# Optimization experiments

Measured on AMD Instinct MI355X. Metric: run time of the kernel, lower is better.

Reference implementation:

```python
import jax, jax.numpy as jnp
import numpy as np

N_HEAD = 12
N_EMBD = 768


def setup_inputs() -> dict:
    key = jax.random.key(0)
    ks = jax.random.split(key, 5)
    B, T, C = 8, 1024, N_EMBD
    x = jax.random.normal(ks[0], (B, T, C), dtype=jnp.float32)
    # c_attn: Linear(C, 3C); c_proj: Linear(C, C). PyTorch Linear: y = x @ W.T + b
    s = 1.0 / np.sqrt(C)
    W_attn = jax.random.uniform(ks[1], (3 * C, C), minval=-s, maxval=s, dtype=jnp.float32)
    b_attn = jax.random.uniform(ks[2], (3 * C,), minval=-s, maxval=s, dtype=jnp.float32)
    W_proj = jax.random.uniform(ks[3], (C, C), minval=-s, maxval=s, dtype=jnp.float32)
    b_proj = jax.random.uniform(ks[4], (C,), minval=-s, maxval=s, dtype=jnp.float32)
    return {"x": x, "W_attn": W_attn, "b_attn": b_attn, "W_proj": W_proj, "b_proj": b_proj}


def reference(x, W_attn, b_attn, W_proj, b_proj):
    B, T, C = x.shape
    H = N_HEAD
    hs = C // H  # head size
    qkv = x @ W_attn.T + b_attn  # [B, T, 3C]
    q, k, v = jnp.split(qkv, 3, axis=2)
    # [B, T, H, hs] -> [B, H, T, hs]
    q = q.reshape(B, T, H, hs).transpose(0, 2, 1, 3)
    k = k.reshape(B, T, H, hs).transpose(0, 2, 1, 3)
    v = v.reshape(B, T, H, hs).transpose(0, 2, 1, 3)
    att = jnp.einsum('bhqd,bhkd->bhqk', q, k) * (1.0 / np.sqrt(hs))
    causal = jnp.tril(jnp.ones((T, T), dtype=bool))
    att = jnp.where(causal, att, -jnp.inf)
    att = jax.nn.softmax(att, axis=-1)
    y = jnp.einsum('bhqk,bhkd->bhqd', att, v)  # [B, H, T, hs]
    y = y.transpose(0, 2, 1, 3).reshape(B, T, C)
    return y @ W_proj.T + b_proj
```

## Files before the change

kernel.cpp:

```cpp
#include <hip/hip_runtime.h>

typedef unsigned short u16;
typedef __attribute__((ext_vector_type(8))) __bf16 bf16x8;
typedef __attribute__((ext_vector_type(4))) float f32x4;
typedef __attribute__((ext_vector_type(4))) int i32x4;

#define MFMA16(a, b, c) __builtin_amdgcn_mfma_f32_16x16x32_bf16(a, b, c, 0, 0, 0)

__device__ __forceinline__ u16 f2b(float f) {
  __bf16 h = (__bf16)f;
  return __builtin_bit_cast(u16, h);
}

__device__ __forceinline__ void gl_lds16(const void* g, void* l) {
  __builtin_amdgcn_global_load_lds(
      (const __attribute__((address_space(1))) void*)g,
      (__attribute__((address_space(3))) void*)l, 16, 0, 0);
}

__device__ __forceinline__ bf16x8 ldf(const void* p) {
  return __builtin_bit_cast(bf16x8, *(const i32x4*)p);
}

__global__ __launch_bounds__(256) void cvt3_kernel(
    const float4* __restrict__ a, ushort4* __restrict__ oa, int na4,
    const float4* __restrict__ b, ushort4* __restrict__ ob, int nb4,
    const float4* __restrict__ c, ushort4* __restrict__ oc, int nc4) {
  const int step = gridDim.x * blockDim.x;
  const int t0 = blockIdx.x * blockDim.x + threadIdx.x;
  for (int i = t0; i < na4; i += step) {
    float4 v = a[i];
    ushort4 o; o.x = f2b(v.x); o.y = f2b(v.y); o.z = f2b(v.z); o.w = f2b(v.w);
    oa[i] = o;
  }
  for (int i = t0; i < nb4; i += step) {
    float4 v = b[i];
    ushort4 o; o.x = f2b(v.x); o.y = f2b(v.y); o.z = f2b(v.z); o.w = f2b(v.w);
    ob[i] = o;
  }
  for (int i = t0; i < nc4; i += step) {
    float4 v = c[i];
    ushort4 o; o.x = f2b(v.x); o.y = f2b(v.y); o.z = f2b(v.z); o.w = f2b(v.w);
    oc[i] = o;
  }
}

template <int EPI>
__global__ __launch_bounds__(512, 4) void gemm3(
    const u16* __restrict__ A, const u16* __restrict__ B,
    const float* __restrict__ bias, int M, int N, int K,
    u16* __restrict__ q_s, u16* __restrict__ k_s, u16* __restrict__ vt_s,
    float* __restrict__ outf) {
  constexpr int BM = 128, BN = 192;
  constexpr int NR = BN / 64;
  constexpr int IA = BM / 64;
  constexpr int IB = BN / 64;
  __shared__ __align__(16) u16 As[BM * 64];
  __shared__ __align__(16) u16 Bs[BN * 64];
  const int tid = threadIdx.x;
  const int w = tid >> 6, l = tid & 63;
  const int lo = l & 15, hi = l >> 4;
  const int wr = w >> 2, wc = w & 3;
  const int nwg = gridDim.x * gridDim.y;
  int bid = blockIdx.y * gridDim.x + blockIdx.x;
  bid = (bid & 7) * (nwg >> 3) + (bid >> 3);
  const int bm0 = (bid / gridDim.x) * BM;
  const int bn0 = (bid % gridDim.x) * BN;
  const size_t Kb = (size_t)K * 2;
  const char* Ab = (const char*)A;
  const char* Bb = (const char*)B;
  const int lrow8 = l >> 3;
  const int lcol = (l & 7) * 16;

  f32x4 acc[4][NR] = {};

  for (int kt = 0; kt < K; kt += 64) {
    __syncthreads();
#pragma unroll
    for (int i = 0; i < IA; ++i) {
      int rl = (w * IA + i) * 8 + lrow8;
      int cb = lcol ^ ((rl & 7) << 4);
      gl_lds16(Ab + (size_t)(bm0 + rl) * Kb + kt * 2 + cb,
               (char*)As + (w * IA + i) * 1024);
    }
#pragma unroll
    for (int i = 0; i < IB; ++i) {
      int rl = (w * IB + i) * 8 + lrow8;
      int cb = lcol ^ ((rl & 7) << 4);
      gl_lds16(Bb + (size_t)(bn0 + rl) * Kb + kt * 2 + cb,
               (char*)Bs + (w * IB + i) * 1024);
    }
    __syncthreads();
#pragma unroll
    for (int ks = 0; ks < 2; ++ks) {
      bf16x8 bfr[NR];
#pragma unroll
      for (int nf = 0; nf < NR; ++nf) {
        int r = wc * (NR * 16) + nf * 16 + lo;
        bfr[nf] = ldf((char*)Bs + r * 128 + ((ks * 64 + hi * 16) ^ ((r & 7) << 4)));
      }
#pragma unroll
      for (int mf = 0; mf < 4; ++mf) {
        int r = wr * 64 + mf * 16 + lo;
        bf16x8 afr = ldf((char*)As + r * 128 + ((ks * 64 + hi * 16) ^ ((r & 7) << 4)));
#pragma unroll
        for (int nf = 0; nf < NR; ++nf) acc[mf][nf] = MFMA16(afr, bfr[nf], acc[mf][nf]);
      }
    }
  }

#pragma unroll
  for (int nf = 0; nf < NR; ++nf) {
    int col = bn0 + wc * (NR * 16) + nf * 16 + lo;
    float bv = bias[col];
    if (EPI == 0) {
      int seg = col / 768;
      int cs = col - seg * 768;
      int h = cs >> 6, d = cs & 63;
      u16* dst = (seg == 0) ? q_s : k_s;
#pragma unroll
      for (int mf = 0; mf < 4; ++mf) {
        int m0 = bm0 + wr * 64 + mf * 16 + hi * 4;
        int bb = m0 >> 10, t0 = m0 & 1023;
        size_t bh = (size_t)(bb * 12 + h);
        if (seg < 2) {
#pragma unroll
          for (int r = 0; r < 4; ++r)
            dst[(bh * 1024 + t0 + r) * 64 + d] = f2b(acc[mf][nf][r] + bv);
        } else {
          ushort4 pk;
          pk.x = f2b(acc[mf][nf][0] + bv);
          pk.y = f2b(acc[mf][nf][1] + bv);
          pk.z = f2b(acc[mf][nf][2] + bv);
          pk.w = f2b(acc[mf][nf][3] + bv);
          *(ushort4*)&vt_s[(bh * 64 + d) * 1024 + t0] = pk;
        }
      }
    } else {
#pragma unroll
      for (int mf = 0; mf < 4; ++mf) {
        int m0 = bm0 + wr * 64 + mf * 16 + hi * 4;
#pragma unroll
        for (int r = 0; r < 4; ++r) outf[(size_t)(m0 + r) * N + col] = acc[mf][nf][r] + bv;
      }
    }
  }
}

__global__ __launch_bounds__(256) void attn_kernel(
    const u16* __restrict__ Q, const u16* __restrict__ Kg,
    const u16* __restrict__ Vt, u16* __restrict__ Y) {
  __shared__ __align__(16) u16 Ks[2][64 * 64];
  __shared__ __align__(16) u16 Vs[2][64 * 64];
  __shared__ __align__(16) u16 Ps[4][16 * 64];
  const int tid = threadIdx.x;
  const int w = tid >> 6, l = tid & 63;
  const int lo = l & 15, hi = l >> 4;
  int bid = blockIdx.y * gridDim.x + blockIdx.x;
  bid = (bid & 7) * 96 + (bid >> 3);
  const int bh = bid >> 3;
  const int pr = bid & 7;
  const int b = bh / 12, h = bh % 12;
  const float c1 = 0.125f * 1.44269504f;
  char* pw = (char*)&Ps[w][0];
  const int swl = (lo & 7) << 4;
  const u16* Qb = Q + (size_t)bh * 65536;
  const char* Kbp = (const char*)(Kg + (size_t)bh * 65536);
  const char* Vbp = (const char*)(Vt + (size_t)bh * 65536);

  auto STAGE = [&](int buf, int kb) {
#pragma unroll
    for (int i = 0; i < 2; ++i) {
      int c = w * 2 + i;
      int row = c * 8 + (l >> 3);
      int cb = ((l & 7) * 16) ^ ((row & 7) << 4);
      gl_lds16(Kbp + (size_t)(kb + row) * 128 + cb, (char*)&Ks[buf][0] + c * 1024);
      gl_lds16(Vbp + (size_t)row * 2048 + (size_t)kb * 2 + cb, (char*)&Vs[buf][0] + c * 1024);
    }
  };

  for (int sg = 0; sg < 2; ++sg) {
    const int tile = sg ? (15 - pr) : pr;
    const int q0 = tile * 64 + w * 16;
    const int nt = tile + 1;

    bf16x8 qf[2];
#pragma unroll
    for (int ks = 0; ks < 2; ++ks)
      qf[ks] = ldf(Qb + (size_t)(q0 + lo) * 64 + ks * 32 + hi * 8);

    f32x4 o[4] = {};
    f32x4 mrow, lrow;
#pragma unroll
    for (int r = 0; r < 4; ++r) { mrow[r] = -1e30f; lrow[r] = 0.0f; }

    STAGE(0, 0);
    for (int kt = 0; kt < nt; ++kt) {
      const int cur = kt & 1;
      if (kt + 1 < nt) {
        STAGE(cur ^ 1, (kt + 1) * 64);
        asm volatile("s_waitcnt vmcnt(4)" ::: "memory");
      } else {
        asm volatile("s_waitcnt vmcnt(0)" ::: "memory");
      }
      __builtin_amdgcn_s_barrier();
      __builtin_amdgcn_sched_barrier(0);
      const char* Kt = (const char*)&Ks[cur][0];
      const char* Vv = (const char*)&Vs[cur][0];
      const int kb = kt * 64;

      f32x4 sv[4] = {};
#pragma unroll
      for (int kf = 0; kf < 4; ++kf) {
        int rb = (kf * 16 + lo) * 128;
#pragma unroll
        for (int ks = 0; ks < 2; ++ks)
          sv[kf] = MFMA16(qf[ks], ldf(Kt + rb + ((ks * 64 + hi * 16) ^ swl)), sv[kf]);
      }
      if (kt == nt - 1) {
#pragma unroll
        for (int kf = 0; kf < 4; ++kf)
#pragma unroll
          for (int r = 0; r < 4; ++r) {
            int qrow = q0 + hi * 4 + r;
            int kcol = kb + kf * 16 + lo;
            if (kcol > qrow) sv[kf][r] = -1e30f;
          }
      }
      f32x4 lm = sv[0];
#pragma unroll
      for (int kf = 1; kf < 4; ++kf)
#pragma unroll
        for (int r = 0; r < 4; ++r) lm[r] = fmaxf(lm[r], sv[kf][r]);
      bool need = false;
#pragma unroll
      for (int r = 0; r < 4; ++r) need |= (lm[r] * c1 > mrow[r] + 8.0f);
      if (__any(need)) {
#pragma unroll
        for (int st = 1; st < 16; st <<= 1)
#pragma unroll
          for (int r = 0; r < 4; ++r) lm[r] = fmaxf(lm[r], __shfl_xor(lm[r], st));
        f32x4 al;
#pragma unroll
        for (int r = 0; r < 4; ++r) {
          float Mn = fmaxf(mrow[r], lm[r] * c1);
          al[r] = __builtin_amdgcn_exp2f(mrow[r] - Mn);
          mrow[r] = Mn;
          lrow[r] *= al[r];
        }
#pragma unroll
        for (int nd = 0; nd < 4; ++nd)
#pragma unroll
          for (int r = 0; r < 4; ++r) o[nd][r] *= al[r];
      }
      f32x4 rs = {0.f, 0.f, 0.f, 0.f};
#pragma unroll
      for (int kf = 0; kf < 4; ++kf)
#pragma unroll
        for (int r = 0; r < 4; ++r) {
          float pv = __builtin_amdgcn_exp2f(fmaf(sv[kf][r], c1, -mrow[r]));
          sv[kf][r] = pv;
          rs[r] += pv;
        }
#pragma unroll
      for (int st = 1; st < 16; st <<= 1)
#pragma unroll
        for (int r = 0; r < 4; ++r) rs[r] += __shfl_xor(rs[r], st);
#pragma unroll
      for (int r = 0; r < 4; ++r) lrow[r] += rs[r];
#pragma unroll
      for (int kf = 0; kf < 4; ++kf)
#pragma unroll
        for (int r = 0; r < 4; ++r) {
          int qrow = hi * 4 + r;
          int cb = ((lo + kf * 16) * 2) ^ ((qrow & 7) << 4);
          *(u16*)(pw + qrow * 128 + cb) = f2b(sv[kf][r]);
        }
      bf16x8 pa[2];
#pragma unroll
      for (int ks = 0; ks < 2; ++ks)
        pa[ks] = ldf(pw + lo * 128 + ((ks * 64 + hi * 16) ^ swl));
#pragma unroll
      for (int nd = 0; nd < 4; ++nd) {
        int rb = (nd * 16 + lo) * 128;
#pragma unroll
        for (int ks = 0; ks < 2; ++ks)
          o[nd] = MFMA16(pa[ks], ldf(Vv + rb + ((ks * 64 + hi * 16) ^ swl)), o[nd]);
      }
      __builtin_amdgcn_sched_barrier(0);
      __builtin_amdgcn_s_barrier();
    }

    f32x4 inv;
#pragma unroll
    for (int r = 0; r < 4; ++r) inv[r] = 1.0f / lrow[r];
#pragma unroll
    for (int nd = 0; nd < 4; ++nd)
#pragma unroll
      for (int r = 0; r < 4; ++r) {
        int t = q0 + hi * 4 + r;
        int d = nd * 16 + lo;
        Y[((size_t)b * 1024 + t) * 768 + h * 64 + d] = f2b(o[nd][r] * inv[r]);
      }
  }
}

extern "C" void kernel_launch(void* const* d_in, const int* in_sizes, int n_in,
                              void* d_out, int out_size, void* d_ws, size_t ws_size,
                              hipStream_t stream) {
  const float* x  = (const float*)d_in[0];
  const float* Wa = (const float*)d_in[1];
  const float* ba = (const float*)d_in[2];
  const float* Wp = (const float*)d_in[3];
  const float* bp = (const float*)d_in[4];
  float* out = (float*)d_out;
  char* ws = (char*)d_ws;

  constexpr size_t XB  = 0;
  constexpr size_t WAB = 12582912;
  constexpr size_t WPB = WAB + 3538944;
  constexpr size_t QS  = WPB + 1179648;
  constexpr size_t KS  = QS + 12582912;
  constexpr size_t VTS = KS + 12582912;
  constexpr size_t YB  = VTS + 12582912;

  u16* xb  = (u16*)(ws + XB);
  u16* wab = (u16*)(ws + WAB);
  u16* wpb = (u16*)(ws + WPB);
  u16* qs  = (u16*)(ws + QS);
  u16* ks  = (u16*)(ws + KS);
  u16* vts = (u16*)(ws + VTS);
  u16* yb  = (u16*)(ws + YB);

  cvt3_kernel<<<2048, 256, 0, stream>>>(
      (const float4*)x,  (ushort4*)xb,  8192 * 768 / 4,
      (const float4*)Wa, (ushort4*)wab, 2304 * 768 / 4,
      (const float4*)Wp, (ushort4*)wpb, 768 * 768 / 4);

  gemm3<0><<<dim3(12, 64), 512, 0, stream>>>(xb, wab, ba, 8192, 2304, 768,
                                             qs, ks, vts, nullptr);
  attn_kernel<<<dim3(8, 96), 256, 0, stream>>>(qs, ks, vts, yb);
  gemm3<1><<<dim3(4, 64), 512, 0, stream>>>(yb, wpb, bp, 8192, 768, 768,
                                            nullptr, nullptr, nullptr, out);
}
```

Before: 116.6 us.

## Compute softmax row sums via MFMA, prefetch V, set priorities, shrink proj GEMM tile

In the attention kernel, the row sum of P is now accumulated with an extra MFMA against a ones vector, replacing the exp-sum plus cross-lane shuffle reduction. V fragments are loaded from LDS before the softmax so their latency overlaps it, and s_setprio raises wave priority around the MFMA blocks. The GEMM is templated on BM, and the output projection uses BM=64 with twice as many blocks to fill more CUs. These changes trade extra MFMA work and register pressure for fewer shuffles, and bf16-rounded P now feeds the row sum.

```diff
diff --git a/kernel.cpp b/kernel.cpp
--- a/kernel.cpp
+++ b/kernel.cpp
@@ -45,13 +45,14 @@
   }
 }
 
-template <int EPI>
+template <int BM, int EPI>
 __global__ __launch_bounds__(512, 4) void gemm3(
     const u16* __restrict__ A, const u16* __restrict__ B,
     const float* __restrict__ bias, int M, int N, int K,
     u16* __restrict__ q_s, u16* __restrict__ k_s, u16* __restrict__ vt_s,
     float* __restrict__ outf) {
-  constexpr int BM = 128, BN = 192;
+  constexpr int BN = 192;
+  constexpr int MR = BM / 32;
   constexpr int NR = BN / 64;
   constexpr int IA = BM / 64;
   constexpr int IB = BN / 64;
@@ -72,7 +73,7 @@
   const int lrow8 = l >> 3;
   const int lcol = (l & 7) * 16;
 
-  f32x4 acc[4][NR] = {};
+  f32x4 acc[MR][NR] = {};
 
   for (int kt = 0; kt < K; kt += 64) {
     __syncthreads();
@@ -100,8 +101,8 @@
         bfr[nf] = ldf((char*)Bs + r * 128 + ((ks * 64 + hi * 16) ^ ((r & 7) << 4)));
       }
 #pragma unroll
-      for (int mf = 0; mf < 4; ++mf) {
-        int r = wr * 64 + mf * 16 + lo;
+      for (int mf = 0; mf < MR; ++mf) {
+        int r = wr * (MR * 16) + mf * 16 + lo;
         bf16x8 afr = ldf((char*)As + r * 128 + ((ks * 64 + hi * 16) ^ ((r & 7) << 4)));
 #pragma unroll
         for (int nf = 0; nf < NR; ++nf) acc[mf][nf] = MFMA16(afr, bfr[nf], acc[mf][nf]);
@@ -119,8 +120,8 @@
       int h = cs >> 6, d = cs & 63;
       u16* dst = (seg == 0) ? q_s : k_s;
 #pragma unroll
-      for (int mf = 0; mf < 4; ++mf) {
-        int m0 = bm0 + wr * 64 + mf * 16 + hi * 4;
+      for (int mf = 0; mf < MR; ++mf) {
+        int m0 = bm0 + wr * (MR * 16) + mf * 16 + hi * 4;
         int bb = m0 >> 10, t0 = m0 & 1023;
         size_t bh = (size_t)(bb * 12 + h);
         if (seg < 2) {
@@ -138,8 +139,8 @@
       }
     } else {
 #pragma unroll
-      for (int mf = 0; mf < 4; ++mf) {
-        int m0 = bm0 + wr * 64 + mf * 16 + hi * 4;
+      for (int mf = 0; mf < MR; ++mf) {
+        int m0 = bm0 + wr * (MR * 16) + mf * 16 + hi * 4;
 #pragma unroll
         for (int r = 0; r < 4; ++r) outf[(size_t)(m0 + r) * N + col] = acc[mf][nf][r] + bv;
       }
@@ -168,6 +169,10 @@
   const char* Kbp = (const char*)(Kg + (size_t)bh * 65536);
   const char* Vbp = (const char*)(Vt + (size_t)bh * 65536);
 
+  bf16x8 onesv;
+#pragma unroll
+  for (int j = 0; j < 8; ++j) onesv[j] = (__bf16)1.0f;
+
   auto STAGE = [&](int buf, int kb) {
 #pragma unroll
     for (int i = 0; i < 2; ++i) {
@@ -190,9 +195,9 @@
       qf[ks] = ldf(Qb + (size_t)(q0 + lo) * 64 + ks * 32 + hi * 8);
 
     f32x4 o[4] = {};
-    f32x4 mrow, lrow;
-#pragma unroll
-    for (int r = 0; r < 4; ++r) { mrow[r] = -1e30f; lrow[r] = 0.0f; }
+    f32x4 mrow, lsum;
+#pragma unroll
+    for (int r = 0; r < 4; ++r) { mrow[r] = -1e30f; lsum[r] = 0.0f; }
 
     STAGE(0, 0);
     for (int kt = 0; kt < nt; ++kt) {
@@ -210,12 +215,22 @@
       const int kb = kt * 64;
 
       f32x4 sv[4] = {};
+      __builtin_amdgcn_s_setprio(1);
 #pragma unroll
       for (int kf = 0; kf < 4; ++kf) {
         int rb = (kf * 16 + lo) * 128;
 #pragma unroll
         for (int ks = 0; ks < 2; ++ks)
           sv[kf] = MFMA16(qf[ks], ldf(Kt + rb + ((ks * 64 + hi * 16) ^ swl)), sv[kf]);
+      }
+      __builtin_amdgcn_s_setprio(0);
+      bf16x8 vb[4][2];
+#pragma unroll
+      for (int nd = 0; nd < 4; ++nd) {
+        int rb = (nd * 16 + lo) * 128;
+#pragma unroll
+        for (int ks = 0; ks < 2; ++ks)
+          vb[nd][ks] = ldf(Vv + rb + ((ks * 64 + hi * 16) ^ swl));
       }
       if (kt == nt - 1) {
 #pragma unroll
@@ -246,28 +261,18 @@
           float Mn = fmaxf(mrow[r], lm[r] * c1);
           al[r] = __builtin_amdgcn_exp2f(mrow[r] - Mn);
           mrow[r] = Mn;
-          lrow[r] *= al[r];
+          lsum[r] *= al[r];
         }
 #pragma unroll
         for (int nd = 0; nd < 4; ++nd)
 #pragma unroll
           for (int r = 0; r < 4; ++r) o[nd][r] *= al[r];
       }
-      f32x4 rs = {0.f, 0.f, 0.f, 0.f};
 #pragma unroll
       for (int kf = 0; kf < 4; ++kf)
 #pragma unroll
-        for (int r = 0; r < 4; ++r) {
-          float pv = __builtin_amdgcn_exp2f(fmaf(sv[kf][r], c1, -mrow[r]));
-          sv[kf][r] = pv;
-          rs[r] += pv;
-        }
-#pragma unroll
-      for (int st = 1; st < 16; st <<= 1)
-#pragma unroll
-        for (int r = 0; r < 4; ++r) rs[r] += __shfl_xor(rs[r], st);
-#pragma unroll
-      for (int r = 0; r < 4; ++r) lrow[r] += rs[r];
+        for (int r = 0; r < 4; ++r)
+          sv[kf][r] = __builtin_amdgcn_exp2f(fmaf(sv[kf][r], c1, -mrow[r]));
 #pragma unroll
       for (int kf = 0; kf < 4; ++kf)
 #pragma unroll
@@ -280,20 +285,21 @@
 #pragma unroll
       for (int ks = 0; ks < 2; ++ks)
         pa[ks] = ldf(pw + lo * 128 + ((ks * 64 + hi * 16) ^ swl));
-#pragma unroll
-      for (int nd = 0; nd < 4; ++nd) {
-        int rb = (nd * 16 + lo) * 128;
-#pragma unroll
-        for (int ks = 0; ks < 2; ++ks)
-          o[nd] = MFMA16(pa[ks], ldf(Vv + rb + ((ks * 64 + hi * 16) ^ swl)), o[nd]);
-      }
+      __builtin_amdgcn_s_setprio(1);
+#pragma unroll
+      for (int ks = 0; ks < 2; ++ks) {
+#pragma unroll
+        for (int nd = 0; nd < 4; ++nd) o[nd] = MFMA16(pa[ks], vb[nd][ks], o[nd]);
+        lsum = MFMA16(pa[ks], onesv, lsum);
+      }
+      __builtin_amdgcn_s_setprio(0);
       __builtin_amdgcn_sched_barrier(0);
       __builtin_amdgcn_s_barrier();
     }
 
     f32x4 inv;
 #pragma unroll
-    for (int r = 0; r < 4; ++r) inv[r] = 1.0f / lrow[r];
+    for (int r = 0; r < 4; ++r) inv[r] = 1.0f / lsum[r];
 #pragma unroll
     for (int nd = 0; nd < 4; ++nd)
 #pragma unroll
@@ -337,9 +343,9 @@
       (const float4*)Wa, (ushort4*)wab, 2304 * 768 / 4,
       (const float4*)Wp, (ushort4*)wpb, 768 * 768 / 4);
 
-  gemm3<0><<<dim3(12, 64), 512, 0, stream>>>(xb, wab, ba, 8192, 2304, 768,
-                                             qs, ks, vts, nullptr);
+  gemm3<128, 0><<<dim3(12, 64), 512, 0, stream>>>(xb, wab, ba, 8192, 2304, 768,
+                                                  qs, ks, vts, nullptr);
   attn_kernel<<<dim3(8, 96), 256, 0, stream>>>(qs, ks, vts, yb);
-  gemm3<1><<<dim3(4, 64), 512, 0, stream>>>(yb, wpb, bp, 8192, 768, 768,
-                                            nullptr, nullptr, nullptr, out);
-}
+  gemm3<64, 1><<<dim3(4, 128), 512, 0, stream>>>(yb, wpb, bp, 8192, 768, 768,
+                                                 nullptr, nullptr, nullptr, out);
+}
```

Result: faster. 105.7 us (-9.3%).
